# Kernel tuning notes

Measured on AMD Instinct MI355X. Metric: run time of the kernel, lower is better.

The kernel has to match this reference:

```python
import jax, jax.numpy as jnp
import numpy as np

N_NODES = 50000
N_EDGES = 800000
D = 256
N_LAYERS = 3
BN_EPS = 1e-5


def setup_inputs() -> dict:
    key = jax.random.key(0)
    ks = jax.random.split(key, 7)
    x = jax.random.normal(ks[0], (N_NODES, D), dtype=jnp.float32)
    Wl = jax.random.normal(ks[1], (N_LAYERS, D, D), dtype=jnp.float32)
    bl = jax.random.normal(ks[2], (N_LAYERS, D), dtype=jnp.float32)
    Wr = jax.random.normal(ks[3], (N_LAYERS, D, D), dtype=jnp.float32)
    gamma = jax.random.uniform(ks[4], (N_LAYERS, D), dtype=jnp.float32)
    beta = jax.random.normal(ks[5], (N_LAYERS, D), dtype=jnp.float32)
    edge_index = jax.random.randint(ks[6], (2, N_EDGES), 0, N_NODES, dtype=jnp.int64)
    return {"x": x, "Wl": Wl, "bl": bl, "Wr": Wr, "gamma": gamma,
            "beta": beta, "edge_index": edge_index}


def reference(x, Wl, bl, Wr, gamma, beta, edge_index):
    """3-layer GNN: SAGEConv(mean) -> BatchNorm1d(train) -> ReLU per layer."""
    src = edge_index[0]
    dst = edge_index[1]
    n = x.shape[0]
    # In-degree (mean-aggregation denominator); clamp to avoid div-by-zero.
    deg = jax.ops.segment_sum(jnp.ones((src.shape[0],), dtype=x.dtype), dst,
                              num_segments=n)
    deg = jnp.maximum(deg, 1.0)[:, None]  # [N, 1]
    n_layers = Wl.shape[0]
    for i in range(n_layers):
        # --- SAGEConv: mean-aggregate neighbor messages, then linear ---
        agg = jax.ops.segment_sum(x[src], dst, num_segments=n) / deg  # [N, D]
        h = agg @ Wl[i] + bl[i] + x @ Wr[i]                           # [N, D]
        # --- BatchNorm1d (training mode: batch stats, biased variance) ---
        mu = jnp.mean(h, axis=0)
        var = jnp.mean(jnp.square(h - mu), axis=0)
        h = (h - mu) * jax.lax.rsqrt(var + BN_EPS) * gamma[i] + beta[i]
        # --- ReLU ---
        x = jax.nn.relu(h)
    return x
```

## Files before the change

### kernel.cpp

```cpp
#include <hip/hip_runtime.h>

#define N_NODES 50000
#define N_PAD   50176
#define N_EDGES 800000
#define DIM     256
#define KDIM    512
#define BN_EPS  1e-5f
#define SCAN_NB ((N_NODES + 1023) / 1024)

typedef __attribute__((ext_vector_type(8))) short short8;
typedef __attribute__((ext_vector_type(4))) float floatx4;

__device__ __forceinline__ float bf2f(unsigned short u) {
    return __uint_as_float(((unsigned int)u) << 16);
}
__device__ __forceinline__ unsigned short f2bf(float f) {
    unsigned int b = __float_as_uint(f);
    b = (b + 0x7FFF + ((b >> 16) & 1)) >> 16;
    return (unsigned short)b;
}

__device__ __forceinline__ void gload_lds16(const void* g, void* l) {
    __builtin_amdgcn_global_load_lds(
        (const __attribute__((address_space(1))) unsigned int*)g,
        (__attribute__((address_space(3))) unsigned int*)l, 16, 0, 0);
}


__global__ void k_deg_count(const int* __restrict__ dst, int* __restrict__ degi) {
    int e = blockIdx.x * blockDim.x + threadIdx.x;
    if (e < N_EDGES) atomicAdd(&degi[dst[e]], 1);
}

__global__ void k_scan1(const int* __restrict__ degi, int* __restrict__ off,
                        float* __restrict__ inv_deg, int* __restrict__ bsums) {
    __shared__ int buf[1024];
    int i = blockIdx.x * 1024 + threadIdx.x;
    int v = (i < N_NODES) ? degi[i] : 0;
    if (i < N_NODES) inv_deg[i] = 1.0f / (float)max(v, 1);
    buf[threadIdx.x] = v;
    __syncthreads();
    for (int s = 1; s < 1024; s <<= 1) {
        int t = (threadIdx.x >= s) ? buf[threadIdx.x - s] : 0;
        __syncthreads();
        buf[threadIdx.x] += t;
        __syncthreads();
    }
    if (i < N_NODES) off[i + 1] = buf[threadIdx.x];
    if (threadIdx.x == 1023) bsums[blockIdx.x] = buf[1023];
    if (i == 0) off[0] = 0;
}

__global__ void k_scan2(int* __restrict__ bsums) {
    int t = threadIdx.x;
    int orig = (t < SCAN_NB) ? bsums[t] : 0;
    int v = orig;
    for (int s = 1; s < 64; s <<= 1) {
        int u = __shfl_up(v, s, 64);
        if (t >= s) v += u;
    }
    if (t < SCAN_NB) bsums[t] = v - orig;
}

__global__ void k_scan3(int* __restrict__ off, const int* __restrict__ bsums) {
    int i = blockIdx.x * 1024 + threadIdx.x;
    if (i < N_NODES) off[i + 1] += bsums[blockIdx.x];
}

__global__ void k_fill(const int* __restrict__ src, const int* __restrict__ dst,
                       const int* __restrict__ off, int* __restrict__ cursor,
                       int* __restrict__ csr_src) {
    int e = blockIdx.x * blockDim.x + threadIdx.x;
    if (e < N_EDGES) {
        int d = dst[e];
        int pos = atomicAdd(&cursor[d], 1);
        csr_src[off[d] + pos] = src[e];
    }
}


__global__ void k_prep_w(const float* __restrict__ Wl, const float* __restrict__ Wr,
                         unsigned short* __restrict__ Wcat) {
    int gid = blockIdx.x * blockDim.x + threadIdx.x;
    if (gid >= 3 * DIM * KDIM) return;
    int k = gid & (KDIM - 1);
    int n = (gid >> 9) & (DIM - 1);
    int l = gid >> 17;
    float v = (k < DIM) ? Wl[(size_t)l * DIM * DIM + (size_t)k * DIM + n]
                        : Wr[(size_t)l * DIM * DIM + (size_t)(k - DIM) * DIM + n];
    Wcat[gid] = f2bf(v);
}


__global__ void k_x2bf(const float* __restrict__ x, unsigned short* __restrict__ Acat) {
    size_t i = (size_t)blockIdx.x * blockDim.x + threadIdx.x;
    if (i >= (size_t)N_NODES * (DIM / 4)) return;
    int node = (int)(i >> 6);
    int c = ((int)i & 63) * 4;
    float4 v = ((const float4*)x)[i];
    ushort4 o; o.x = f2bf(v.x); o.y = f2bf(v.y); o.z = f2bf(v.z); o.w = f2bf(v.w);
    *(ushort4*)&Acat[(size_t)node * KDIM + DIM + c] = o;
}


__device__ __forceinline__ void addv(float* a, uint4 v) {
    unsigned int w[4] = {v.x, v.y, v.z, v.w};
    #pragma unroll
    for (int q = 0; q < 4; ++q) {
        a[2 * q + 0] += bf2f((unsigned short)(w[q] & 0xFFFF));
        a[2 * q + 1] += bf2f((unsigned short)(w[q] >> 16));
    }
}

__global__ __launch_bounds__(256) void k_aggregate(
        const unsigned short* __restrict__ Acat_x,
        const int* __restrict__ off,
        const int* __restrict__ csr_src,
        const float* __restrict__ inv_deg,
        unsigned short* __restrict__ Acat_agg) {
    int gid = blockIdx.x * blockDim.x + threadIdx.x;
    int node = gid >> 5;
    int lane = threadIdx.x & 31;
    if (node >= N_NODES) return;
    int beg = off[node], end = off[node + 1];
    float a[8];
    #pragma unroll
    for (int q = 0; q < 8; ++q) a[q] = 0.f;
    const unsigned short* xb = Acat_x + DIM + lane * 8;

    int e = beg;
    for (; e + 8 <= end; e += 8) {
        uint4 v0 = *(const uint4*)(xb + (size_t)csr_src[e + 0] * KDIM);
        uint4 v1 = *(const uint4*)(xb + (size_t)csr_src[e + 1] * KDIM);
        uint4 v2 = *(const uint4*)(xb + (size_t)csr_src[e + 2] * KDIM);
        uint4 v3 = *(const uint4*)(xb + (size_t)csr_src[e + 3] * KDIM);
        uint4 v4 = *(const uint4*)(xb + (size_t)csr_src[e + 4] * KDIM);
        uint4 v5 = *(const uint4*)(xb + (size_t)csr_src[e + 5] * KDIM);
        uint4 v6 = *(const uint4*)(xb + (size_t)csr_src[e + 6] * KDIM);
        uint4 v7 = *(const uint4*)(xb + (size_t)csr_src[e + 7] * KDIM);
        addv(a, v0); addv(a, v1); addv(a, v2); addv(a, v3);
        addv(a, v4); addv(a, v5); addv(a, v6); addv(a, v7);
    }
    for (; e + 4 <= end; e += 4) {
        uint4 v0 = *(const uint4*)(xb + (size_t)csr_src[e + 0] * KDIM);
        uint4 v1 = *(const uint4*)(xb + (size_t)csr_src[e + 1] * KDIM);
        uint4 v2 = *(const uint4*)(xb + (size_t)csr_src[e + 2] * KDIM);
        uint4 v3 = *(const uint4*)(xb + (size_t)csr_src[e + 3] * KDIM);
        addv(a, v0); addv(a, v1); addv(a, v2); addv(a, v3);
    }
    for (; e < end; ++e) {
        uint4 v = *(const uint4*)(xb + (size_t)csr_src[e] * KDIM);
        addv(a, v);
    }

    float inv = inv_deg[node];
    unsigned int w[4];
    #pragma unroll
    for (int q = 0; q < 4; ++q)
        w[q] = (unsigned int)f2bf(a[2 * q] * inv) |
               ((unsigned int)f2bf(a[2 * q + 1] * inv) << 16);
    uint4 o; o.x = w[0]; o.y = w[1]; o.z = w[2]; o.w = w[3];
    *(uint4*)&Acat_agg[(size_t)node * KDIM + lane * 8] = o;
}


__global__ __launch_bounds__(256) void k_gemm_mfma(
        const unsigned short* __restrict__ A,
        const unsigned short* __restrict__ Bt,
        const float* __restrict__ bias, unsigned short* __restrict__ H,
        float* __restrict__ ssum, float* __restrict__ ssq) {
    __shared__ __align__(16) short Alds[2][128 * 32];
    __shared__ __align__(16) short Blds[2][128 * 32];
    int tid = threadIdx.x;
    int wid = tid >> 6;
    int lane = tid & 63;
    int wm = wid >> 1, wn = wid & 1;
    int brow = blockIdx.x * 128;
    int bcol = blockIdx.y * 128;

    floatx4 acc[4][4];
    #pragma unroll
    for (int i = 0; i < 4; ++i)
        #pragma unroll
        for (int j = 0; j < 4; ++j) acc[i][j] = (floatx4){0.f, 0.f, 0.f, 0.f};

    int st_r0 = (lane >> 2);
    int st_s  = lane & 3;
    int rb = lane & 15;
    int k16r = lane >> 4;

    auto stage = [&](int buf, int kt) {
        int k0 = kt * 32;
        #pragma unroll
        for (int q = 0; q < 2; ++q) {
            int c = wid * 2 + q;
            int r = c * 16 + st_r0;
            int k16 = (st_s - (r >> 1)) & 3;
            gload_lds16(A + (size_t)(brow + r) * KDIM + k0 + k16 * 8, &Alds[buf][c * 512]);
            gload_lds16(Bt + (size_t)(bcol + r) * KDIM + k0 + k16 * 8, &Blds[buf][c * 512]);
        }
    };

    stage(0, 0);
    __syncthreads();
    int cur = 0;
    for (int kt = 0; kt < KDIM / 32; ++kt) {
        if (kt + 1 < KDIM / 32) stage(cur ^ 1, kt + 1);

        short8 af[4], bfr[4];
        #pragma unroll
        for (int i = 0; i < 4; ++i) {
            int ra = wm * 64 + i * 16 + rb;
            int sa = (k16r + (ra >> 1)) & 3;
            af[i] = *(const short8*)&Alds[cur][ra * 32 + sa * 8];
            int rc = wn * 64 + i * 16 + rb;
            int sc = (k16r + (rc >> 1)) & 3;
            bfr[i] = *(const short8*)&Blds[cur][rc * 32 + sc * 8];
        }
        #pragma unroll
        for (int i = 0; i < 4; ++i)
            #pragma unroll
            for (int j = 0; j < 4; ++j)
                acc[i][j] = __builtin_amdgcn_mfma_f32_16x16x32_bf16(
                    af[i], bfr[j], acc[i][j], 0, 0, 0);
        __syncthreads();
        cur ^= 1;
    }

    int rg = lane >> 4;
    #pragma unroll
    for (int j = 0; j < 4; ++j) {
        int col = bcol + wn * 64 + j * 16 + rb;
        float bv = bias[col];
        float s = 0.f, s2 = 0.f;
        #pragma unroll
        for (int i = 0; i < 4; ++i) {
            #pragma unroll
            for (int q = 0; q < 4; ++q) {
                int row = brow + wm * 64 + i * 16 + rg * 4 + q;
                float o = acc[i][j][q] + bv;
                unsigned short hb = f2bf(o);
                if (row < N_NODES) {
                    H[(size_t)row * DIM + col] = hb;
                    float of = bf2f(hb);
                    s += of;
                    s2 = fmaf(of, of, s2);
                }
            }
        }
        s  += __shfl_xor(s, 16);
        s  += __shfl_xor(s, 32);
        s2 += __shfl_xor(s2, 16);
        s2 += __shfl_xor(s2, 32);
        if (rg == 0) {
            atomicAdd(&ssum[col], s);
            atomicAdd(&ssq[col], s2);
        }
    }
}


__global__ void k_norm_relu(const unsigned short* __restrict__ H,
                            const float* __restrict__ ssum,
                            const float* __restrict__ ssq,
                            const float* __restrict__ gamma,
                            const float* __restrict__ beta,
                            float* __restrict__ outF,
                            unsigned short* __restrict__ Acat, int last) {
    __shared__ float sc[DIM], sh[DIM];
    {
        int c = threadIdx.x;
        float mu  = ssum[c] * (1.0f / N_NODES);
        float var = ssq[c] * (1.0f / N_NODES) - mu * mu;
        float rstd = rsqrtf(var + BN_EPS);
        float s = rstd * gamma[c];
        sc[c] = s;
        sh[c] = beta[c] - mu * s;
    }
    __syncthreads();
    size_t total8 = (size_t)N_NODES * DIM / 8;
    for (size_t i = (size_t)blockIdx.x * blockDim.x + threadIdx.x; i < total8;
         i += (size_t)gridDim.x * blockDim.x) {
        uint4 raw = ((const uint4*)H)[i];
        int node = (int)(i >> 5);
        int c = ((int)i & 31) * 8;
        unsigned int w[4] = {raw.x, raw.y, raw.z, raw.w};
        float o[8];
        #pragma unroll
        for (int q = 0; q < 4; ++q) {
            float lo = bf2f((unsigned short)(w[q] & 0xFFFF));
            float hi = bf2f((unsigned short)(w[q] >> 16));
            o[q * 2 + 0] = fmaxf(fmaf(lo, sc[c + q * 2 + 0], sh[c + q * 2 + 0]), 0.f);
            o[q * 2 + 1] = fmaxf(fmaf(hi, sc[c + q * 2 + 1], sh[c + q * 2 + 1]), 0.f);
        }
        if (last) {
            float4 f0 = make_float4(o[0], o[1], o[2], o[3]);
            float4 f1 = make_float4(o[4], o[5], o[6], o[7]);
            *(float4*)(outF + (size_t)node * DIM + c)     = f0;
            *(float4*)(outF + (size_t)node * DIM + c + 4) = f1;
        } else {
            uint4 u;
            unsigned int uw[4];
            #pragma unroll
            for (int q = 0; q < 4; ++q)
                uw[q] = (unsigned int)f2bf(o[q * 2 + 0]) |
                        ((unsigned int)f2bf(o[q * 2 + 1]) << 16);
            u.x = uw[0]; u.y = uw[1]; u.z = uw[2]; u.w = uw[3];
            *(uint4*)&Acat[(size_t)node * KDIM + DIM + c] = u;
        }
    }
}


extern "C" void kernel_launch(void* const* d_in, const int* in_sizes, int n_in,
                              void* d_out, int out_size, void* d_ws, size_t ws_size,
                              hipStream_t stream) {
    const float* x0    = (const float*)d_in[0];
    const float* Wl    = (const float*)d_in[1];
    const float* bl    = (const float*)d_in[2];
    const float* Wr    = (const float*)d_in[3];
    const float* gamma = (const float*)d_in[4];
    const float* beta  = (const float*)d_in[5];
    const int*   ei    = (const int*)d_in[6];
    const int* e_src = ei;
    const int* e_dst = ei + N_EDGES;

    char* ws = (char*)d_ws;
    size_t off = 0;
    auto alloc = [&](size_t bytes) { char* p = ws + off; off = (off + bytes + 255) & ~(size_t)255; return p; };
    unsigned short* Acat = (unsigned short*)alloc((size_t)N_PAD * KDIM * 2);
    unsigned short* Hbuf = (unsigned short*)alloc((size_t)N_PAD * DIM * 2);
    unsigned short* Wcat = (unsigned short*)alloc((size_t)3 * DIM * KDIM * 2);
    int*   csr_src = (int*)alloc((size_t)N_EDGES * 4);
    int*   csr_off = (int*)alloc((size_t)(N_NODES + 1) * 4);
    int*   degi    = (int*)alloc((size_t)N_NODES * 4);
    int*   cursor  = (int*)alloc((size_t)N_NODES * 4);
    int*   bsums   = (int*)alloc((size_t)SCAN_NB * 4);
    float* inv_deg = (float*)alloc((size_t)N_NODES * 4);
    float* stats   = (float*)alloc((size_t)3 * 2 * DIM * 4);
    (void)ws_size;

    hipMemsetAsync(degi, 0, (size_t)N_NODES * 4, stream);
    hipMemsetAsync(cursor, 0, (size_t)N_NODES * 4, stream);
    hipMemsetAsync(stats, 0, (size_t)3 * 2 * DIM * 4, stream);

    int eb = (N_EDGES + 255) / 256;
    k_deg_count<<<eb, 256, 0, stream>>>(e_dst, degi);
    k_scan1<<<SCAN_NB, 1024, 0, stream>>>(degi, csr_off, inv_deg, bsums);
    k_scan2<<<1, 64, 0, stream>>>(bsums);
    k_scan3<<<SCAN_NB, 1024, 0, stream>>>(csr_off, bsums);
    k_fill<<<eb, 256, 0, stream>>>(e_src, e_dst, csr_off, cursor, csr_src);
    k_prep_w<<<(3 * DIM * KDIM + 255) / 256, 256, 0, stream>>>(Wl, Wr, Wcat);
    k_x2bf<<<(N_NODES * (DIM / 4) + 255) / 256, 256, 0, stream>>>(x0, Acat);

    for (int l = 0; l < 3; ++l) {
        float* ssum_l = stats + (size_t)l * 2 * DIM;
        float* ssq_l  = ssum_l + DIM;
        k_aggregate<<<(N_NODES * 32 + 255) / 256, 256, 0, stream>>>(
            Acat, csr_off, csr_src, inv_deg, Acat);
        k_gemm_mfma<<<dim3((N_NODES + 127) / 128, DIM / 128), 256, 0, stream>>>(
            Acat, Wcat + (size_t)l * DIM * KDIM, bl + (size_t)l * DIM, Hbuf, ssum_l, ssq_l);
        k_norm_relu<<<2048, 256, 0, stream>>>(Hbuf, ssum_l, ssq_l,
                                              gamma + (size_t)l * DIM, beta + (size_t)l * DIM,
                                              (float*)d_out, Acat, (l == 2) ? 1 : 0);
    }
}
```

Before: 584.9 us.

## Restructure GEMM to single-buffer BK=64 tiles and fuse setup kernels

The GEMM moves from a double-buffered BK=32 pipeline to a single-buffered BK=64 tile with an XOR swizzle, so it runs half as many K iterations and barriers but no longer overlaps loads with MFMA. Several setup kernels are merged to cut launch count: the scan2 and scan3 kernels become one, weight prep and x conversion become one, and three memsets become one. The norm kernel is split into bf16 and fp32-output variants to remove a runtime branch, and the aggregate kernel gets a minimum-occupancy launch bound. Losing load/compute overlap in the GEMM could offset the savings.

Result: slower. 703.3 us (+20.2%).

```diff
diff --git a/kernel.cpp b/kernel.cpp
--- a/kernel.cpp
+++ b/kernel.cpp
@@ -7,6 +7,7 @@
 #define KDIM    512
 #define BN_EPS  1e-5f
 #define SCAN_NB ((N_NODES + 1023) / 1024)
+#define NT      (KDIM / 64)
 
 typedef __attribute__((ext_vector_type(8))) short short8;
 typedef __attribute__((ext_vector_type(4))) float floatx4;
@@ -51,20 +52,17 @@
     if (i == 0) off[0] = 0;
 }
 
-__global__ void k_scan2(int* __restrict__ bsums) {
+__global__ void k_scan3(int* __restrict__ off, const int* __restrict__ bsums) {
+    __shared__ int boff;
     int t = threadIdx.x;
-    int orig = (t < SCAN_NB) ? bsums[t] : 0;
-    int v = orig;
-    for (int s = 1; s < 64; s <<= 1) {
-        int u = __shfl_up(v, s, 64);
-        if (t >= s) v += u;
-    }
-    if (t < SCAN_NB) bsums[t] = v - orig;
-}
-
-__global__ void k_scan3(int* __restrict__ off, const int* __restrict__ bsums) {
+    if (t < 64) {
+        int v = (t < SCAN_NB && t < (int)blockIdx.x) ? bsums[t] : 0;
+        for (int s = 32; s >= 1; s >>= 1) v += __shfl_xor(v, s, 64);
+        if (t == 0) boff = v;
+    }
+    __syncthreads();
     int i = blockIdx.x * 1024 + threadIdx.x;
-    if (i < N_NODES) off[i + 1] += bsums[blockIdx.x];
+    if (i < N_NODES) off[i + 1] += boff;
 }
 
 __global__ void k_fill(const int* __restrict__ src, const int* __restrict__ dst,
@@ -79,27 +77,30 @@
 }
 
 
-__global__ void k_prep_w(const float* __restrict__ Wl, const float* __restrict__ Wr,
-                         unsigned short* __restrict__ Wcat) {
+#define PREPW_N (3 * DIM * KDIM)
+#define X2BF_N  (N_NODES * (DIM / 4))
+
+__global__ void k_prep(const float* __restrict__ Wl, const float* __restrict__ Wr,
+                       unsigned short* __restrict__ Wcat,
+                       const float* __restrict__ x, unsigned short* __restrict__ Acat) {
     int gid = blockIdx.x * blockDim.x + threadIdx.x;
-    if (gid >= 3 * DIM * KDIM) return;
-    int k = gid & (KDIM - 1);
-    int n = (gid >> 9) & (DIM - 1);
-    int l = gid >> 17;
-    float v = (k < DIM) ? Wl[(size_t)l * DIM * DIM + (size_t)k * DIM + n]
-                        : Wr[(size_t)l * DIM * DIM + (size_t)(k - DIM) * DIM + n];
-    Wcat[gid] = f2bf(v);
-}
-
-
-__global__ void k_x2bf(const float* __restrict__ x, unsigned short* __restrict__ Acat) {
-    size_t i = (size_t)blockIdx.x * blockDim.x + threadIdx.x;
-    if (i >= (size_t)N_NODES * (DIM / 4)) return;
-    int node = (int)(i >> 6);
-    int c = ((int)i & 63) * 4;
-    float4 v = ((const float4*)x)[i];
-    ushort4 o; o.x = f2bf(v.x); o.y = f2bf(v.y); o.z = f2bf(v.z); o.w = f2bf(v.w);
-    *(ushort4*)&Acat[(size_t)node * KDIM + DIM + c] = o;
+    if (gid < PREPW_N) {
+        int k = gid & (KDIM - 1);
+        int n = (gid >> 9) & (DIM - 1);
+        int l = gid >> 17;
+        float v = (k < DIM) ? Wl[(size_t)l * DIM * DIM + (size_t)k * DIM + n]
+                            : Wr[(size_t)l * DIM * DIM + (size_t)(k - DIM) * DIM + n];
+        Wcat[gid] = f2bf(v);
+        return;
+    }
+    int xid = gid - PREPW_N;
+    if (xid < X2BF_N) {
+        int node = xid >> 6;
+        int c = (xid & 63) * 4;
+        float4 v = ((const float4*)x)[xid];
+        ushort4 o; o.x = f2bf(v.x); o.y = f2bf(v.y); o.z = f2bf(v.z); o.w = f2bf(v.w);
+        *(ushort4*)&Acat[(size_t)node * KDIM + DIM + c] = o;
+    }
 }
 
 
@@ -112,7 +113,7 @@
     }
 }
 
-__global__ __launch_bounds__(256) void k_aggregate(
+__global__ __launch_bounds__(256, 8) void k_aggregate(
         const unsigned short* __restrict__ Acat_x,
         const int* __restrict__ off,
         const int* __restrict__ csr_src,
@@ -169,8 +170,8 @@
         const unsigned short* __restrict__ Bt,
         const float* __restrict__ bias, unsigned short* __restrict__ H,
         float* __restrict__ ssum, float* __restrict__ ssq) {
-    __shared__ __align__(16) short Alds[2][128 * 32];
-    __shared__ __align__(16) short Blds[2][128 * 32];
+    __shared__ __align__(16) short Alds[128 * 64];
+    __shared__ __align__(16) short Blds[128 * 64];
     int tid = threadIdx.x;
     int wid = tid >> 6;
     int lane = tid & 63;
@@ -184,47 +185,44 @@
         #pragma unroll
         for (int j = 0; j < 4; ++j) acc[i][j] = (floatx4){0.f, 0.f, 0.f, 0.f};
 
-    int st_r0 = (lane >> 2);
-    int st_s  = lane & 3;
+    int st_row = lane >> 3;
+    int st_s   = lane & 7;
+    int sg_st  = st_s ^ st_row;
     int rb = lane & 15;
     int k16r = lane >> 4;
 
-    auto stage = [&](int buf, int kt) {
-        int k0 = kt * 32;
-        #pragma unroll
-        for (int q = 0; q < 2; ++q) {
-            int c = wid * 2 + q;
-            int r = c * 16 + st_r0;
-            int k16 = (st_s - (r >> 1)) & 3;
-            gload_lds16(A + (size_t)(brow + r) * KDIM + k0 + k16 * 8, &Alds[buf][c * 512]);
-            gload_lds16(Bt + (size_t)(bcol + r) * KDIM + k0 + k16 * 8, &Blds[buf][c * 512]);
-        }
-    };
-
-    stage(0, 0);
-    __syncthreads();
-    int cur = 0;
-    for (int kt = 0; kt < KDIM / 32; ++kt) {
-        if (kt + 1 < KDIM / 32) stage(cur ^ 1, kt + 1);
-
-        short8 af[4], bfr[4];
-        #pragma unroll
-        for (int i = 0; i < 4; ++i) {
-            int ra = wm * 64 + i * 16 + rb;
-            int sa = (k16r + (ra >> 1)) & 3;
-            af[i] = *(const short8*)&Alds[cur][ra * 32 + sa * 8];
-            int rc = wn * 64 + i * 16 + rb;
-            int sc = (k16r + (rc >> 1)) & 3;
-            bfr[i] = *(const short8*)&Blds[cur][rc * 32 + sc * 8];
-        }
-        #pragma unroll
-        for (int i = 0; i < 4; ++i)
+    for (int kt = 0; kt < NT; ++kt) {
+        int k0 = kt * 64;
+        #pragma unroll
+        for (int q = 0; q < 4; ++q) {
+            int c = wid * 4 + q;
+            int r = c * 8 + st_row;
+            gload_lds16(A + (size_t)(brow + r) * KDIM + k0 + sg_st * 8,
+                        &Alds[c * 512]);
+            gload_lds16(Bt + (size_t)(bcol + r) * KDIM + k0 + sg_st * 8,
+                        &Blds[c * 512]);
+        }
+        __syncthreads();
+
+        #pragma unroll
+        for (int kk = 0; kk < 2; ++kk) {
+            short8 af[4], bfr[4];
             #pragma unroll
-            for (int j = 0; j < 4; ++j)
-                acc[i][j] = __builtin_amdgcn_mfma_f32_16x16x32_bf16(
-                    af[i], bfr[j], acc[i][j], 0, 0, 0);
+            for (int i = 0; i < 4; ++i) {
+                int ra = wm * 64 + i * 16 + rb;
+                int s_st = (kk * 4 + k16r) ^ (rb & 7);
+                af[i] = *(const short8*)&Alds[ra * 64 + s_st * 8];
+                int rc = wn * 64 + i * 16 + rb;
+                bfr[i] = *(const short8*)&Blds[rc * 64 + s_st * 8];
+            }
+            #pragma unroll
+            for (int i = 0; i < 4; ++i)
+                #pragma unroll
+                for (int j = 0; j < 4; ++j)
+                    acc[i][j] = __builtin_amdgcn_mfma_f32_16x16x32_bf16(
+                        af[i], bfr[j], acc[i][j], 0, 0, 0);
+        }
         __syncthreads();
-        cur ^= 1;
     }
 
     int rg = lane >> 4;
@@ -260,13 +258,10 @@
 }
 
 
-__global__ void k_norm_relu(const unsigned short* __restrict__ H,
-                            const float* __restrict__ ssum,
-                            const float* __restrict__ ssq,
-                            const float* __restrict__ gamma,
-                            const float* __restrict__ beta,
-                            float* __restrict__ outF,
-                            unsigned short* __restrict__ Acat, int last) {
+__global__ void k_norm(const unsigned short* __restrict__ H,
+                       const float* __restrict__ ssum, const float* __restrict__ ssq,
+                       const float* __restrict__ gamma, const float* __restrict__ beta,
+                       unsigned short* __restrict__ Acat) {
     __shared__ float sc[DIM], sh[DIM];
     {
         int c = threadIdx.x;
@@ -285,6 +280,43 @@
         int node = (int)(i >> 5);
         int c = ((int)i & 31) * 8;
         unsigned int w[4] = {raw.x, raw.y, raw.z, raw.w};
+        unsigned int uw[4];
+        #pragma unroll
+        for (int q = 0; q < 4; ++q) {
+            float lo = bf2f((unsigned short)(w[q] & 0xFFFF));
+            float hi = bf2f((unsigned short)(w[q] >> 16));
+            lo = fmaxf(fmaf(lo, sc[c + q * 2 + 0], sh[c + q * 2 + 0]), 0.f);
+            hi = fmaxf(fmaf(hi, sc[c + q * 2 + 1], sh[c + q * 2 + 1]), 0.f);
+            uw[q] = (unsigned int)f2bf(lo) | ((unsigned int)f2bf(hi) << 16);
+        }
+        uint4 u; u.x = uw[0]; u.y = uw[1]; u.z = uw[2]; u.w = uw[3];
+        *(uint4*)&Acat[(size_t)node * KDIM + DIM + c] = u;
+    }
+}
+
+
+__global__ void k_out(const unsigned short* __restrict__ H,
+                      const float* __restrict__ ssum, const float* __restrict__ ssq,
+                      const float* __restrict__ gamma, const float* __restrict__ beta,
+                      float* __restrict__ outF) {
+    __shared__ float sc[DIM], sh[DIM];
+    {
+        int c = threadIdx.x;
+        float mu  = ssum[c] * (1.0f / N_NODES);
+        float var = ssq[c] * (1.0f / N_NODES) - mu * mu;
+        float rstd = rsqrtf(var + BN_EPS);
+        float s = rstd * gamma[c];
+        sc[c] = s;
+        sh[c] = beta[c] - mu * s;
+    }
+    __syncthreads();
+    size_t total8 = (size_t)N_NODES * DIM / 8;
+    for (size_t i = (size_t)blockIdx.x * blockDim.x + threadIdx.x; i < total8;
+         i += (size_t)gridDim.x * blockDim.x) {
+        uint4 raw = ((const uint4*)H)[i];
+        int node = (int)(i >> 5);
+        int c = ((int)i & 31) * 8;
+        unsigned int w[4] = {raw.x, raw.y, raw.z, raw.w};
         float o[8];
         #pragma unroll
         for (int q = 0; q < 4; ++q) {
@@ -293,21 +325,10 @@
             o[q * 2 + 0] = fmaxf(fmaf(lo, sc[c + q * 2 + 0], sh[c + q * 2 + 0]), 0.f);
             o[q * 2 + 1] = fmaxf(fmaf(hi, sc[c + q * 2 + 1], sh[c + q * 2 + 1]), 0.f);
         }
-        if (last) {
-            float4 f0 = make_float4(o[0], o[1], o[2], o[3]);
-            float4 f1 = make_float4(o[4], o[5], o[6], o[7]);
-            *(float4*)(outF + (size_t)node * DIM + c)     = f0;
-            *(float4*)(outF + (size_t)node * DIM + c + 4) = f1;
-        } else {
-            uint4 u;
-            unsigned int uw[4];
-            #pragma unroll
-            for (int q = 0; q < 4; ++q)
-                uw[q] = (unsigned int)f2bf(o[q * 2 + 0]) |
-                        ((unsigned int)f2bf(o[q * 2 + 1]) << 16);
-            u.x = uw[0]; u.y = uw[1]; u.z = uw[2]; u.w = uw[3];
-            *(uint4*)&Acat[(size_t)node * KDIM + DIM + c] = u;
-        }
+        float4 f0 = make_float4(o[0], o[1], o[2], o[3]);
+        float4 f1 = make_float4(o[4], o[5], o[6], o[7]);
+        *(float4*)(outF + (size_t)node * DIM + c)     = f0;
+        *(float4*)(outF + (size_t)node * DIM + c + 4) = f1;
     }
 }
 
@@ -333,35 +354,37 @@
     unsigned short* Wcat = (unsigned short*)alloc((size_t)3 * DIM * KDIM * 2);
     int*   csr_src = (int*)alloc((size_t)N_EDGES * 4);
     int*   csr_off = (int*)alloc((size_t)(N_NODES + 1) * 4);
-    int*   degi    = (int*)alloc((size_t)N_NODES * 4);
-    int*   cursor  = (int*)alloc((size_t)N_NODES * 4);
+    char*  zbase   = alloc((size_t)50176 * 4 * 2 + 6144);
+    int*   degi    = (int*)zbase;
+    int*   cursor  = (int*)(zbase + 50176 * 4);
+    float* stats   = (float*)(zbase + 50176 * 4 * 2);
     int*   bsums   = (int*)alloc((size_t)SCAN_NB * 4);
     float* inv_deg = (float*)alloc((size_t)N_NODES * 4);
-    float* stats   = (float*)alloc((size_t)3 * 2 * DIM * 4);
     (void)ws_size;
 
-    hipMemsetAsync(degi, 0, (size_t)N_NODES * 4, stream);
-    hipMemsetAsync(cursor, 0, (size_t)N_NODES * 4, stream);
-    hipMemsetAsync(stats, 0, (size_t)3 * 2 * DIM * 4, stream);
+    hipMemsetAsync(zbase, 0, (size_t)50176 * 4 * 2 + 6144, stream);
 
     int eb = (N_EDGES + 255) / 256;
     k_deg_count<<<eb, 256, 0, stream>>>(e_dst, degi);
     k_scan1<<<SCAN_NB, 1024, 0, stream>>>(degi, csr_off, inv_deg, bsums);
-    k_scan2<<<1, 64, 0, stream>>>(bsums);
     k_scan3<<<SCAN_NB, 1024, 0, stream>>>(csr_off, bsums);
     k_fill<<<eb, 256, 0, stream>>>(e_src, e_dst, csr_off, cursor, csr_src);
-    k_prep_w<<<(3 * DIM * KDIM + 255) / 256, 256, 0, stream>>>(Wl, Wr, Wcat);
-    k_x2bf<<<(N_NODES * (DIM / 4) + 255) / 256, 256, 0, stream>>>(x0, Acat);
-
+    k_prep<<<(PREPW_N + X2BF_N + 255) / 256, 256, 0, stream>>>(Wl, Wr, Wcat, x0, Acat);
+
+    int ab = (N_NODES * 32 + 255) / 256;
     for (int l = 0; l < 3; ++l) {
         float* ssum_l = stats + (size_t)l * 2 * DIM;
         float* ssq_l  = ssum_l + DIM;
-        k_aggregate<<<(N_NODES * 32 + 255) / 256, 256, 0, stream>>>(
-            Acat, csr_off, csr_src, inv_deg, Acat);
-        k_gemm_mfma<<<dim3((N_NODES + 127) / 128, DIM / 128), 256, 0, stream>>>(
-            Acat, Wcat + (size_t)l * DIM * KDIM, bl + (size_t)l * DIM, Hbuf, ssum_l, ssq_l);
-        k_norm_relu<<<2048, 256, 0, stream>>>(Hbuf, ssum_l, ssq_l,
-                                              gamma + (size_t)l * DIM, beta + (size_t)l * DIM,
-                                              (float*)d_out, Acat, (l == 2) ? 1 : 0);
-    }
-}
+        k_aggregate<<<ab, 256, 0, stream>>>(Acat, csr_off, csr_src, inv_deg, Acat);
+        k_gemm_mfma<<<dim3(N_PAD / 128, DIM / 128), 256, 0, stream>>>(
+            Acat, Wcat + (size_t)l * DIM * KDIM, bl + (size_t)l * DIM, Hbuf,
+            ssum_l, ssq_l);
+        if (l < 2)
+            k_norm<<<2048, 256, 0, stream>>>(Hbuf, ssum_l, ssq_l,
+                                             gamma + (size_t)l * DIM,
+                                             beta + (size_t)l * DIM, Acat);
+    }
+    float* ssum2 = stats + (size_t)2 * 2 * DIM;
+    k_out<<<2048, 256, 0, stream>>>(Hbuf, ssum2, ssum2 + DIM,
+                                    gamma + 2 * DIM, beta + 2 * DIM, (float*)d_out);
+}
```
